# Performance work log

Measured on AMD Instinct MI355X. Metric: run time of the kernel, lower is better.

## Reference

```python
import jax, jax.numpy as jnp
import numpy as np

D_MODEL, D_FF, H, B, S = 1024, 4096, 16, 4, 2048
D_K = D_MODEL // H
EPS = 1e-5
NEG = -1e9


def _custom_ln(x, alpha, bias):
    # torch: mean, std (unbiased, N-1), alpha*(x-mean)/(std+eps)+bias; alpha/bias scalars
    mean = jnp.mean(x, axis=-1, keepdims=True)
    n = x.shape[-1]
    var = jnp.sum((x - mean) ** 2, axis=-1, keepdims=True) / (n - 1)
    std = jnp.sqrt(var)
    return alpha * (x - mean) / (std + EPS) + bias


def setup_inputs() -> dict:
    key = jax.random.key(0)
    ks = jax.random.split(key, 12)
    sc_d = 1.0 / np.sqrt(D_MODEL)
    sc_f = 1.0 / np.sqrt(D_FF)
    inp = {
        "x": jax.random.normal(ks[0], (B, S, D_MODEL), jnp.float32),
        "src_mask": jnp.ones((B, 1, 1, S), jnp.int32),
        "wq": jax.random.normal(ks[1], (D_MODEL, D_MODEL), jnp.float32) * sc_d,
        "bq": jnp.zeros((D_MODEL,), jnp.float32),
        "wk": jax.random.normal(ks[2], (D_MODEL, D_MODEL), jnp.float32) * sc_d,
        "bk": jnp.zeros((D_MODEL,), jnp.float32),
        "wv": jax.random.normal(ks[3], (D_MODEL, D_MODEL), jnp.float32) * sc_d,
        "bv": jnp.zeros((D_MODEL,), jnp.float32),
        "wo": jax.random.normal(ks[4], (D_MODEL, D_MODEL), jnp.float32) * sc_d,
        "bo": jnp.zeros((D_MODEL,), jnp.float32),
        "w1": jax.random.normal(ks[5], (D_MODEL, D_FF), jnp.float32) * sc_d,
        "b1": jnp.zeros((D_FF,), jnp.float32),
        "w2": jax.random.normal(ks[6], (D_FF, D_MODEL), jnp.float32) * sc_f,
        "b2": jnp.zeros((D_MODEL,), jnp.float32),
        "ln1_a": jnp.ones((1,), jnp.float32),
        "ln1_b": jnp.zeros((1,), jnp.float32),
        "ln2_a": jnp.ones((1,), jnp.float32),
        "ln2_b": jnp.zeros((1,), jnp.float32),
    }
    return inp


def _attention(xn, src_mask, wq, bq, wk, bk, wv, bv, wo, bo):
    q = (xn @ wq + bq).reshape(B, S, H, D_K).transpose(0, 2, 1, 3)  # [B,H,S,Dk]
    k = (xn @ wk + bk).reshape(B, S, H, D_K).transpose(0, 2, 1, 3)
    v = (xn @ wv + bv).reshape(B, S, H, D_K).transpose(0, 2, 1, 3)
    scores = jnp.einsum("bhqd,bhkd->bhqk", q, k) / np.sqrt(D_K)
    scores = jnp.where(src_mask == 0, NEG, scores)
    attn = jax.nn.softmax(scores, axis=-1)
    ctx = jnp.einsum("bhqk,bhkd->bhqd", attn, v)
    ctx = ctx.transpose(0, 2, 1, 3).reshape(B, S, D_MODEL)
    return ctx @ wo + bo


def reference(x, src_mask, wq, bq, wk, bk, wv, bv, wo, bo,
              w1, b1, w2, b2, ln1_a, ln1_b, ln2_a, ln2_b):
    # pre-LN attention residual (dropout=0 -> identity)
    xn = _custom_ln(x, ln1_a, ln1_b)
    x = x + _attention(xn, src_mask, wq, bq, wk, bk, wv, bv, wo, bo)
    # pre-LN FFN residual
    xn = _custom_ln(x, ln2_a, ln2_b)
    ff = jax.nn.relu(xn @ w1 + b1) @ w2 + b2
    return x + ff
```

## Files before the change

### kernel.cpp

```cpp
#include <hip/hip_runtime.h>

typedef unsigned short u16;
typedef __bf16 bf16x8 __attribute__((ext_vector_type(8)));
typedef float f32x4 __attribute__((ext_vector_type(4)));

__device__ __forceinline__ u16 f2bf(float f) {
  unsigned u = __builtin_bit_cast(unsigned, f);
  unsigned lsb = (u >> 16) & 1u;
  u += 0x7fffu + lsb;
  return (u16)(u >> 16);
}

__device__ __forceinline__ unsigned cvt_pk_bf16(float lo, float hi) {
  unsigned r;
  asm("v_cvt_pk_bf16_f32 %0, %1, %2" : "=v"(r) : "v"(lo), "v"(hi));
  return r;
}

__device__ __forceinline__ void gld_lds16(const u16* g, u16* l) {
  __builtin_amdgcn_global_load_lds(
      (__attribute__((address_space(1))) void*)g,
      (__attribute__((address_space(3))) void*)l, 16, 0, 0);
}

__global__ __launch_bounds__(256) void ln_kernel(
    const float* __restrict__ x, u16* __restrict__ out,
    const float* __restrict__ alpha_p, const float* __restrict__ beta_p) {
  const int row = blockIdx.x;
  const int t = threadIdx.x;
  const float4 v = reinterpret_cast<const float4*>(x + (size_t)row * 1024)[t];
  float s = v.x + v.y + v.z + v.w;
  float sq = v.x * v.x + v.y * v.y + v.z * v.z + v.w * v.w;
#pragma unroll
  for (int off = 32; off > 0; off >>= 1) {
    s += __shfl_down(s, off);
    sq += __shfl_down(sq, off);
  }
  __shared__ float red[8];
  const int w = t >> 6;
  if ((t & 63) == 0) { red[w] = s; red[4 + w] = sq; }
  __syncthreads();
  const float ts = red[0] + red[1] + red[2] + red[3];
  const float tq = red[4] + red[5] + red[6] + red[7];
  const float mean = ts * (1.0f / 1024.0f);
  float var = (tq - ts * mean) * (1.0f / 1023.0f);
  var = fmaxf(var, 0.0f);
  const float rden = 1.0f / (sqrtf(var) + 1e-5f);
  const float a = alpha_p[0], bb = beta_p[0];
  uint2 ov;
  ov.x = cvt_pk_bf16(a * (v.x - mean) * rden + bb, a * (v.y - mean) * rden + bb);
  ov.y = cvt_pk_bf16(a * (v.z - mean) * rden + bb, a * (v.w - mean) * rden + bb);
  reinterpret_cast<uint2*>(out + (size_t)row * 1024)[t] = ov;
}

__global__ __launch_bounds__(256) void wcvt_t(
    const float* __restrict__ w, u16* __restrict__ wt, int K, int N, float scale) {
  __shared__ float tile[32][33];
  const int n0 = blockIdx.x * 32, k0 = blockIdx.y * 32;
  const int tx = threadIdx.x, ty = threadIdx.y;
#pragma unroll
  for (int i = 0; i < 4; ++i)
    tile[ty + i * 8][tx] = w[(size_t)(k0 + ty + i * 8) * N + n0 + tx];
  __syncthreads();
#pragma unroll
  for (int i = 0; i < 4; ++i)
    wt[(size_t)(n0 + ty + i * 8) * K + k0 + tx] = f2bf(tile[tx][ty + i * 8] * scale);
}

__global__ __launch_bounds__(256) void pack_bias(
    const float* __restrict__ a, const float* __restrict__ b,
    const float* __restrict__ c, float* __restrict__ o, float qscale) {
  const int i = blockIdx.x * 256 + threadIdx.x;
  o[i] = (i < 1024) ? a[i] * qscale : ((i < 2048) ? b[i - 1024] : c[i - 2048]);
}

__global__ __launch_bounds__(256) void mk_mbias(
    const int* __restrict__ mask, float* __restrict__ mb, int* __restrict__ flags) {
  const int b = blockIdx.x, t = threadIdx.x;
  __shared__ int bad;
  if (t == 0) bad = 0;
  __syncthreads();
  int loc = 0;
#pragma unroll
  for (int i = 0; i < 8; ++i) {
    const int idx = b * 2048 + t * 8 + i;
    const int mv = mask[idx];
    mb[idx] = mv ? 0.f : -1.4427e9f;
    loc |= (mv == 0);
  }
  if (loc) atomicOr(&bad, 1);
  __syncthreads();
  if (t == 0) flags[b] = !bad;
}

template <int EPI>
__global__ __launch_bounds__(256) void gemm_bt(
    const u16* __restrict__ A, const u16* __restrict__ Bt,
    const float* __restrict__ bias, const float* __restrict__ res,
    void* __restrict__ Cout, u16* __restrict__ vt, int M, int N, int K) {
  __shared__ u16 As[128 * 32];
  __shared__ u16 Bs[128 * 32];
  const int tid = threadIdx.x;
  const int l = tid & 63;
  const int w = tid >> 6;
  const int wr = w >> 1, wc = w & 1;
  const int gx = gridDim.x;
  int id = blockIdx.y * gx + blockIdx.x;
  const int nwg = gx * gridDim.y;
  id = (id & 7) * (nwg >> 3) + (id >> 3);
  const int n0 = (id % gx) * 128;
  const int m0 = (id / gx) * 128;
  const int lr = l & 15, lk = (l >> 4) * 8;

  f32x4 acc[4][4];
#pragma unroll
  for (int i = 0; i < 4; ++i)
#pragma unroll
    for (int j = 0; j < 4; ++j) acc[i][j] = f32x4{0.f, 0.f, 0.f, 0.f};

  const int srow = tid >> 2;
  const int scol = (tid & 3) * 8;
  const u16* gA0 = A + (size_t)(m0 + srow) * K + scol;
  const u16* gA1 = A + (size_t)(m0 + 64 + srow) * K + scol;
  const u16* gB0 = Bt + (size_t)(n0 + srow) * K + scol;
  const u16* gB1 = Bt + (size_t)(n0 + 64 + srow) * K + scol;
  u16* lA0 = &As[tid * 8];
  u16* lA1 = &As[2048 + tid * 8];
  u16* lB0 = &Bs[tid * 8];
  u16* lB1 = &Bs[2048 + tid * 8];

  for (int k0 = 0; k0 < K; k0 += 32) {
    gld_lds16(gA0 + k0, lA0);
    gld_lds16(gA1 + k0, lA1);
    gld_lds16(gB0 + k0, lB0);
    gld_lds16(gB1 + k0, lB1);
    __syncthreads();
    bf16x8 a[4], b[4];
#pragma unroll
    for (int mf = 0; mf < 4; ++mf)
      a[mf] = *reinterpret_cast<const bf16x8*>(&As[(wr * 64 + mf * 16 + lr) * 32 + lk]);
#pragma unroll
    for (int nf = 0; nf < 4; ++nf)
      b[nf] = *reinterpret_cast<const bf16x8*>(&Bs[(wc * 64 + nf * 16 + lr) * 32 + lk]);
#pragma unroll
    for (int mf = 0; mf < 4; ++mf)
#pragma unroll
      for (int nf = 0; nf < 4; ++nf)
        acc[mf][nf] = __builtin_amdgcn_mfma_f32_16x16x32_bf16(a[mf], b[nf], acc[mf][nf], 0, 0, 0);
    __syncthreads();
  }

  if (EPI == 3 && n0 >= 2048) {
#pragma unroll
    for (int mf = 0; mf < 4; ++mf) {
#pragma unroll
      for (int nf = 0; nf < 4; ++nf) {
        const int col = n0 + wc * 64 + nf * 16 + lr;
        const float bv = bias[col];
        const int row0 = m0 + wr * 64 + mf * 16 + (l >> 4) * 4;
        const int bb = row0 >> 11, s0 = row0 & 2047;
        const int d = col - 2048;
        uint2 pv;
        pv.x = cvt_pk_bf16(acc[mf][nf][0] + bv, acc[mf][nf][1] + bv);
        pv.y = cvt_pk_bf16(acc[mf][nf][2] + bv, acc[mf][nf][3] + bv);
        *reinterpret_cast<uint2*>(vt + ((size_t)bb * 1024 + d) * 2048 + s0) = pv;
      }
    }
    return;
  }

#pragma unroll
  for (int mf = 0; mf < 4; ++mf) {
#pragma unroll
    for (int nf = 0; nf < 4; ++nf) {
      const int col = n0 + wc * 64 + nf * 16 + lr;
      const float bv = bias[col];
#pragma unroll
      for (int j = 0; j < 4; ++j) {
        const int row = m0 + wr * 64 + mf * 16 + (l >> 4) * 4 + j;
        const size_t idx = (size_t)row * N + col;
        const float vv = acc[mf][nf][j] + bv;
        if (EPI == 0 || EPI == 3)
          ((u16*)Cout)[idx] = f2bf(vv);
        else if (EPI == 1)
          ((float*)Cout)[idx] = vv + res[idx];
        else
          ((u16*)Cout)[idx] = f2bf(fmaxf(vv, 0.f));
      }
    }
  }
}

__global__ __launch_bounds__(256, 4) void attn_fwd4(
    const u16* __restrict__ qkv, const u16* __restrict__ vt,
    const float* __restrict__ mbias, const int* __restrict__ flags,
    u16* __restrict__ ctx) {
  __shared__ u16 Ks[2][64 * 64];
  __shared__ u16 Vs[2][64 * 64];
  const int tid = threadIdx.x;
  const int l = tid & 63;
  const int w = tid >> 6;
  const int b = blockIdx.y >> 4, h = blockIdx.y & 15;
  const int r0 = blockIdx.x * 128 + w * 32;
  const int lr = l & 15, lg = l >> 4;

  const u16* qb = qkv + (size_t)b * 2048 * 3072 + h * 64;
  const u16* kp = qb + 1024;
  const u16* vb = vt + ((size_t)b * 1024 + h * 64) * 2048;
  const float* mb = mbias + (size_t)b * 2048;
  const int allLive = flags[b];

  bf16x8 qf[2][2];
#pragma unroll
  for (int m = 0; m < 2; ++m)
#pragma unroll
    for (int ks = 0; ks < 2; ++ks)
      qf[m][ks] = *reinterpret_cast<const bf16x8*>(
          qb + (size_t)(r0 + m * 16 + lr) * 3072 + ks * 32 + lg * 8);

  float mrun[2] = {-1e30f, -1e30f};
  float lrun[2] = {0.f, 0.f};
  f32x4 o[2][4];
#pragma unroll
  for (int m = 0; m < 2; ++m)
#pragma unroll
    for (int d = 0; d < 4; ++d) o[m][d] = f32x4{0.f, 0.f, 0.f, 0.f};

  const u16* kS[2];
  const u16* vS[2];
#pragma unroll
  for (int i = 0; i < 2; ++i) {
    const int ci = tid + i * 256;
    const int row = ci >> 3, cc = ci & 7;
    const int sc = cc ^ (row & 7);
    kS[i] = kp + (size_t)row * 3072 + sc * 8;
    vS[i] = vb + (size_t)row * 2048 + sc * 8;
  }
#pragma unroll
  for (int i = 0; i < 2; ++i) {
    const int ci8 = (tid + i * 256) * 8;
    gld_lds16(kS[i], &Ks[0][ci8]);
    gld_lds16(vS[i], &Vs[0][ci8]);
  }
  asm volatile("s_waitcnt vmcnt(0)" ::: "memory");
  __syncthreads();

  union U8 { unsigned u[4]; bf16x8 v; };

  int cur = 0;
  for (int t = 0; t < 32; ++t) {
    const int kb0 = t * 64;
    if (t + 1 < 32) {
      const int nb = kb0 + 64;
#pragma unroll
      for (int i = 0; i < 2; ++i) {
        const int ci8 = (tid + i * 256) * 8;
        gld_lds16(kS[i] + (size_t)nb * 3072, &Ks[cur ^ 1][ci8]);
        gld_lds16(vS[i] + nb, &Vs[cur ^ 1][ci8]);
      }
    }

    f32x4 st[2][4];
    __builtin_amdgcn_s_setprio(1);
#pragma unroll
    for (int cf = 0; cf < 4; ++cf) {
      const int krow = cf * 16 + lr;
      const int ch0 = lg ^ (krow & 7);
      const int ch1 = (4 + lg) ^ (krow & 7);
      const bf16x8 kf0 = *reinterpret_cast<const bf16x8*>(&Ks[cur][krow * 64 + ch0 * 8]);
      const bf16x8 kf1 = *reinterpret_cast<const bf16x8*>(&Ks[cur][krow * 64 + ch1 * 8]);
#pragma unroll
      for (int m = 0; m < 2; ++m) {
        f32x4 acc = __builtin_amdgcn_mfma_f32_16x16x32_bf16(kf0, qf[m][0],
                                                            f32x4{0.f, 0.f, 0.f, 0.f}, 0, 0, 0);
        st[m][cf] = __builtin_amdgcn_mfma_f32_16x16x32_bf16(kf1, qf[m][1], acc, 0, 0, 0);
      }
    }
    __builtin_amdgcn_s_setprio(0);

    if (!allLive) {
#pragma unroll
      for (int cf = 0; cf < 4; ++cf) {
        const float4 m4 = *reinterpret_cast<const float4*>(mb + kb0 + cf * 16 + lg * 4);
#pragma unroll
        for (int m = 0; m < 2; ++m) {
          st[m][cf][0] += m4.x;
          st[m][cf][1] += m4.y;
          st[m][cf][2] += m4.z;
          st[m][cf][3] += m4.w;
        }
      }
    }

    bf16x8 paA[2], paB[2];
#pragma unroll
    for (int m = 0; m < 2; ++m) {
      float pm = fmaxf(fmaxf(st[m][0][0], st[m][0][1]), fmaxf(st[m][0][2], st[m][0][3]));
#pragma unroll
      for (int cf = 1; cf < 4; ++cf)
        pm = fmaxf(pm, fmaxf(fmaxf(st[m][cf][0], st[m][cf][1]),
                             fmaxf(st[m][cf][2], st[m][cf][3])));
      pm = fmaxf(pm, __shfl_xor(pm, 16));
      pm = fmaxf(pm, __shfl_xor(pm, 32));
      if (__any(pm > mrun[m] + 8.f)) {
        const float mn = fmaxf(mrun[m], pm);
        const float corr = exp2f(mrun[m] - mn);
        mrun[m] = mn;
        lrun[m] *= corr;
#pragma unroll
        for (int d = 0; d < 4; ++d)
#pragma unroll
          for (int j = 0; j < 4; ++j) o[m][d][j] *= corr;
      }
      float rs = 0.f;
#pragma unroll
      for (int cf = 0; cf < 4; ++cf)
#pragma unroll
        for (int j = 0; j < 4; ++j) {
          const float p = exp2f(st[m][cf][j] - mrun[m]);
          st[m][cf][j] = p;
          rs += p;
        }
      rs += __shfl_xor(rs, 16);
      rs += __shfl_xor(rs, 32);
      lrun[m] += rs;

      unsigned pk[4][2];
#pragma unroll
      for (int cf = 0; cf < 4; ++cf)
#pragma unroll
        for (int wp = 0; wp < 2; ++wp)
          pk[cf][wp] = cvt_pk_bf16(st[m][cf][2 * wp], st[m][cf][2 * wp + 1]);

      U8 a0, a1;
#pragma unroll
      for (int c = 0; c < 2; ++c) {
        const int src = lr + 16 * ((2 * lg + c) & 3);
#pragma unroll
        for (int wp = 0; wp < 2; ++wp) {
          const int v00 = __shfl((int)pk[0][wp], src);
          const int v01 = __shfl((int)pk[1][wp], src);
          const int v10 = __shfl((int)pk[2][wp], src);
          const int v11 = __shfl((int)pk[3][wp], src);
          a0.u[2 * c + wp] = (unsigned)((lg < 2) ? v00 : v01);
          a1.u[2 * c + wp] = (unsigned)((lg < 2) ? v10 : v11);
        }
      }
      paA[m] = a0.v;
      paB[m] = a1.v;
    }

    __builtin_amdgcn_s_setprio(1);
#pragma unroll
    for (int df = 0; df < 4; ++df) {
      const int vrow = df * 16 + lr;
      const int ch0 = lg ^ (vrow & 7);
      const int ch1 = (4 + lg) ^ (vrow & 7);
      const bf16x8 vf0 = *reinterpret_cast<const bf16x8*>(&Vs[cur][vrow * 64 + ch0 * 8]);
      const bf16x8 vf1 = *reinterpret_cast<const bf16x8*>(&Vs[cur][vrow * 64 + ch1 * 8]);
#pragma unroll
      for (int m = 0; m < 2; ++m) {
        o[m][df] = __builtin_amdgcn_mfma_f32_16x16x32_bf16(vf0, paA[m], o[m][df], 0, 0, 0);
        o[m][df] = __builtin_amdgcn_mfma_f32_16x16x32_bf16(vf1, paB[m], o[m][df], 0, 0, 0);
      }
    }
    __builtin_amdgcn_s_setprio(0);

    asm volatile("s_waitcnt vmcnt(0)" ::: "memory");
    __syncthreads();
    cur ^= 1;
  }

#pragma unroll
  for (int m = 0; m < 2; ++m) {
    const float rdiv = 1.f / lrun[m];
    const size_t rowbase = ((size_t)b * 2048 + r0 + m * 16 + lr) * 1024 + h * 64;
#pragma unroll
    for (int df = 0; df < 4; ++df) {
      uint2 s4;
      s4.x = cvt_pk_bf16(o[m][df][0] * rdiv, o[m][df][1] * rdiv);
      s4.y = cvt_pk_bf16(o[m][df][2] * rdiv, o[m][df][3] * rdiv);
      *reinterpret_cast<uint2*>(ctx + rowbase + df * 16 + lg * 4) = s4;
    }
  }
}

extern "C" void kernel_launch(void* const* d_in, const int* in_sizes, int n_in,
                              void* d_out, int out_size, void* d_ws, size_t ws_size,
                              hipStream_t stream) {
  const float* x = (const float*)d_in[0];
  const int* mask = (const int*)d_in[1];
  const float* wq = (const float*)d_in[2];
  const float* bq = (const float*)d_in[3];
  const float* wk = (const float*)d_in[4];
  const float* bk = (const float*)d_in[5];
  const float* wv = (const float*)d_in[6];
  const float* bv = (const float*)d_in[7];
  const float* wo = (const float*)d_in[8];
  const float* bo = (const float*)d_in[9];
  const float* w1 = (const float*)d_in[10];
  const float* b1 = (const float*)d_in[11];
  const float* w2 = (const float*)d_in[12];
  const float* b2 = (const float*)d_in[13];
  const float* ln1a = (const float*)d_in[14];
  const float* ln1b = (const float*)d_in[15];
  const float* ln2a = (const float*)d_in[16];
  const float* ln2b = (const float*)d_in[17];

  const float SCL2 = 0.125f * 1.4426950408889634f;

  char* ws = (char*)d_ws;
  const size_t MB = 1024ull * 1024ull;
  u16* WTQKV = (u16*)(ws + 0 * MB);
  u16* WTO = (u16*)(ws + 6 * MB);
  u16* W1T = (u16*)(ws + 8 * MB);
  u16* W2T = (u16*)(ws + 16 * MB);
  float* BQKV = (float*)(ws + 24 * MB);
  float* MBIAS = (float*)(ws + 24 * MB + 65536);
  int* FLAGS = (int*)(ws + 24 * MB + 131072);
  u16* QKV = (u16*)(ws + 25 * MB);
  u16* VT = (u16*)(ws + 73 * MB);
  u16* XN = (u16*)(ws + 89 * MB);
  u16* CTX = (u16*)(ws + 105 * MB);
  float* X2 = (float*)(ws + 25 * MB);
  u16* XN2 = (u16*)(ws + 57 * MB);
  u16* H1 = (u16*)(ws + 73 * MB);

  dim3 bt(32, 8);
  wcvt_t<<<dim3(32, 32), bt, 0, stream>>>(wq, WTQKV, 1024, 1024, SCL2);
  wcvt_t<<<dim3(32, 32), bt, 0, stream>>>(wk, WTQKV + 1024 * 1024, 1024, 1024, 1.f);
  wcvt_t<<<dim3(32, 32), bt, 0, stream>>>(wv, WTQKV + 2048 * 1024, 1024, 1024, 1.f);
  wcvt_t<<<dim3(32, 32), bt, 0, stream>>>(wo, WTO, 1024, 1024, 1.f);
  wcvt_t<<<dim3(128, 32), bt, 0, stream>>>(w1, W1T, 1024, 4096, 1.f);
  wcvt_t<<<dim3(32, 128), bt, 0, stream>>>(w2, W2T, 4096, 1024, 1.f);
  pack_bias<<<dim3(12), 256, 0, stream>>>(bq, bk, bv, BQKV, SCL2);
  mk_mbias<<<dim3(4), 256, 0, stream>>>(mask, MBIAS, FLAGS);

  ln_kernel<<<8192, 256, 0, stream>>>(x, XN, ln1a, ln1b);
  gemm_bt<3><<<dim3(24, 64), 256, 0, stream>>>(XN, WTQKV, BQKV, nullptr, QKV, VT, 8192, 3072, 1024);
  attn_fwd4<<<dim3(16, 64), 256, 0, stream>>>(QKV, VT, MBIAS, FLAGS, CTX);
  gemm_bt<1><<<dim3(8, 64), 256, 0, stream>>>(CTX, WTO, bo, x, X2, nullptr, 8192, 1024, 1024);
  ln_kernel<<<8192, 256, 0, stream>>>(X2, XN2, ln2a, ln2b);
  gemm_bt<2><<<dim3(32, 64), 256, 0, stream>>>(XN2, W1T, b1, nullptr, H1, nullptr, 8192, 4096, 1024);
  gemm_bt<1><<<dim3(8, 64), 256, 0, stream>>>(H1, W2T, b2, X2, (float*)d_out, nullptr, 8192, 1024, 4096);
}
```

Baseline: 506.9 us.

## Halve attention and N=1024 GEMM tiles and swizzle attention block order

The attention kernel now gives each wave 16 query rows instead of 32, so blocks cover 64 rows and twice as many blocks launch. Block ids are remapped so that neighbouring blocks share the same batch-head for K/V cache reuse. The GEMM gains a BM template parameter, and the two N=1024 GEMMs use 64-row tiles to double their grid and fill more compute units. The cost is that each K/V tile and B tile loaded into shared memory is reused across fewer rows, which raises load traffic per MFMA.

```diff
diff --git a/kernel.cpp b/kernel.cpp
--- a/kernel.cpp
+++ b/kernel.cpp
@@ -93,12 +93,13 @@
   if (t == 0) flags[b] = !bad;
 }
 
-template <int EPI>
+template <int EPI, int BM>
 __global__ __launch_bounds__(256) void gemm_bt(
     const u16* __restrict__ A, const u16* __restrict__ Bt,
     const float* __restrict__ bias, const float* __restrict__ res,
     void* __restrict__ Cout, u16* __restrict__ vt, int M, int N, int K) {
-  __shared__ u16 As[128 * 32];
+  constexpr int MF = BM / 32;
+  __shared__ u16 As[BM * 32];
   __shared__ u16 Bs[128 * 32];
   const int tid = threadIdx.x;
   const int l = tid & 63;
@@ -109,12 +110,12 @@
   const int nwg = gx * gridDim.y;
   id = (id & 7) * (nwg >> 3) + (id >> 3);
   const int n0 = (id % gx) * 128;
-  const int m0 = (id / gx) * 128;
+  const int m0 = (id / gx) * BM;
   const int lr = l & 15, lk = (l >> 4) * 8;
 
-  f32x4 acc[4][4];
-#pragma unroll
-  for (int i = 0; i < 4; ++i)
+  f32x4 acc[MF][4];
+#pragma unroll
+  for (int i = 0; i < MF; ++i)
 #pragma unroll
     for (int j = 0; j < 4; ++j) acc[i][j] = f32x4{0.f, 0.f, 0.f, 0.f};
 
@@ -131,19 +132,19 @@
 
   for (int k0 = 0; k0 < K; k0 += 32) {
     gld_lds16(gA0 + k0, lA0);
-    gld_lds16(gA1 + k0, lA1);
+    if constexpr (BM == 128) gld_lds16(gA1 + k0, lA1);
     gld_lds16(gB0 + k0, lB0);
     gld_lds16(gB1 + k0, lB1);
     __syncthreads();
-    bf16x8 a[4], b[4];
-#pragma unroll
-    for (int mf = 0; mf < 4; ++mf)
-      a[mf] = *reinterpret_cast<const bf16x8*>(&As[(wr * 64 + mf * 16 + lr) * 32 + lk]);
+    bf16x8 a[MF], b[4];
+#pragma unroll
+    for (int mf = 0; mf < MF; ++mf)
+      a[mf] = *reinterpret_cast<const bf16x8*>(&As[(wr * (BM / 2) + mf * 16 + lr) * 32 + lk]);
 #pragma unroll
     for (int nf = 0; nf < 4; ++nf)
       b[nf] = *reinterpret_cast<const bf16x8*>(&Bs[(wc * 64 + nf * 16 + lr) * 32 + lk]);
 #pragma unroll
-    for (int mf = 0; mf < 4; ++mf)
+    for (int mf = 0; mf < MF; ++mf)
 #pragma unroll
       for (int nf = 0; nf < 4; ++nf)
         acc[mf][nf] = __builtin_amdgcn_mfma_f32_16x16x32_bf16(a[mf], b[nf], acc[mf][nf], 0, 0, 0);
@@ -152,12 +153,12 @@
 
   if (EPI == 3 && n0 >= 2048) {
 #pragma unroll
-    for (int mf = 0; mf < 4; ++mf) {
+    for (int mf = 0; mf < MF; ++mf) {
 #pragma unroll
       for (int nf = 0; nf < 4; ++nf) {
         const int col = n0 + wc * 64 + nf * 16 + lr;
         const float bv = bias[col];
-        const int row0 = m0 + wr * 64 + mf * 16 + (l >> 4) * 4;
+        const int row0 = m0 + wr * (BM / 2) + mf * 16 + (l >> 4) * 4;
         const int bb = row0 >> 11, s0 = row0 & 2047;
         const int d = col - 2048;
         uint2 pv;
@@ -170,14 +171,14 @@
   }
 
 #pragma unroll
-  for (int mf = 0; mf < 4; ++mf) {
+  for (int mf = 0; mf < MF; ++mf) {
 #pragma unroll
     for (int nf = 0; nf < 4; ++nf) {
       const int col = n0 + wc * 64 + nf * 16 + lr;
       const float bv = bias[col];
 #pragma unroll
       for (int j = 0; j < 4; ++j) {
-        const int row = m0 + wr * 64 + mf * 16 + (l >> 4) * 4 + j;
+        const int row = m0 + wr * (BM / 2) + mf * 16 + (l >> 4) * 4 + j;
         const size_t idx = (size_t)row * N + col;
         const float vv = acc[mf][nf][j] + bv;
         if (EPI == 0 || EPI == 3)
@@ -191,7 +192,7 @@
   }
 }
 
-__global__ __launch_bounds__(256, 4) void attn_fwd4(
+__global__ __launch_bounds__(256, 4) void attn_fwd5(
     const u16* __restrict__ qkv, const u16* __restrict__ vt,
     const float* __restrict__ mbias, const int* __restrict__ flags,
     u16* __restrict__ ctx) {
@@ -200,8 +201,11 @@
   const int tid = threadIdx.x;
   const int l = tid & 63;
   const int w = tid >> 6;
-  const int b = blockIdx.y >> 4, h = blockIdx.y & 15;
-  const int r0 = blockIdx.x * 128 + w * 32;
+  const int p = blockIdx.y * 32 + blockIdx.x;
+  const int bh = (p & 7) * 8 + (p >> 8);
+  const int qx = (p >> 3) & 31;
+  const int b = bh >> 4, h = bh & 15;
+  const int r0 = qx * 64 + w * 16;
   const int lr = l & 15, lg = l >> 4;
 
   const u16* qb = qkv + (size_t)b * 2048 * 3072 + h * 64;
@@ -210,21 +214,17 @@
   const float* mb = mbias + (size_t)b * 2048;
   const int allLive = flags[b];
 
-  bf16x8 qf[2][2];
-#pragma unroll
-  for (int m = 0; m < 2; ++m)
-#pragma unroll
-    for (int ks = 0; ks < 2; ++ks)
-      qf[m][ks] = *reinterpret_cast<const bf16x8*>(
-          qb + (size_t)(r0 + m * 16 + lr) * 3072 + ks * 32 + lg * 8);
-
-  float mrun[2] = {-1e30f, -1e30f};
-  float lrun[2] = {0.f, 0.f};
-  f32x4 o[2][4];
-#pragma unroll
-  for (int m = 0; m < 2; ++m)
-#pragma unroll
-    for (int d = 0; d < 4; ++d) o[m][d] = f32x4{0.f, 0.f, 0.f, 0.f};
+  bf16x8 qf[2];
+#pragma unroll
+  for (int ks = 0; ks < 2; ++ks)
+    qf[ks] = *reinterpret_cast<const bf16x8*>(
+        qb + (size_t)(r0 + lr) * 3072 + ks * 32 + lg * 8);
+
+  float mrun = -1e30f;
+  float lrun = 0.f;
+  f32x4 o[4];
+#pragma unroll
+  for (int d = 0; d < 4; ++d) o[d] = f32x4{0.f, 0.f, 0.f, 0.f};
 
   const u16* kS[2];
   const u16* vS[2];
@@ -260,7 +260,7 @@
       }
     }
 
-    f32x4 st[2][4];
+    f32x4 st[4];
     __builtin_amdgcn_s_setprio(1);
 #pragma unroll
     for (int cf = 0; cf < 4; ++cf) {
@@ -269,12 +269,9 @@
       const int ch1 = (4 + lg) ^ (krow & 7);
       const bf16x8 kf0 = *reinterpret_cast<const bf16x8*>(&Ks[cur][krow * 64 + ch0 * 8]);
       const bf16x8 kf1 = *reinterpret_cast<const bf16x8*>(&Ks[cur][krow * 64 + ch1 * 8]);
-#pragma unroll
-      for (int m = 0; m < 2; ++m) {
-        f32x4 acc = __builtin_amdgcn_mfma_f32_16x16x32_bf16(kf0, qf[m][0],
-                                                            f32x4{0.f, 0.f, 0.f, 0.f}, 0, 0, 0);
-        st[m][cf] = __builtin_amdgcn_mfma_f32_16x16x32_bf16(kf1, qf[m][1], acc, 0, 0, 0);
-      }
+      f32x4 acc = __builtin_amdgcn_mfma_f32_16x16x32_bf16(kf0, qf[0],
+                                                          f32x4{0.f, 0.f, 0.f, 0.f}, 0, 0, 0);
+      st[cf] = __builtin_amdgcn_mfma_f32_16x16x32_bf16(kf1, qf[1], acc, 0, 0, 0);
     }
     __builtin_amdgcn_s_setprio(0);
 
@@ -282,73 +279,64 @@
 #pragma unroll
       for (int cf = 0; cf < 4; ++cf) {
         const float4 m4 = *reinterpret_cast<const float4*>(mb + kb0 + cf * 16 + lg * 4);
-#pragma unroll
-        for (int m = 0; m < 2; ++m) {
-          st[m][cf][0] += m4.x;
-          st[m][cf][1] += m4.y;
-          st[m][cf][2] += m4.z;
-          st[m][cf][3] += m4.w;
-        }
-      }
-    }
-
-    bf16x8 paA[2], paB[2];
-#pragma unroll
-    for (int m = 0; m < 2; ++m) {
-      float pm = fmaxf(fmaxf(st[m][0][0], st[m][0][1]), fmaxf(st[m][0][2], st[m][0][3]));
-#pragma unroll
-      for (int cf = 1; cf < 4; ++cf)
-        pm = fmaxf(pm, fmaxf(fmaxf(st[m][cf][0], st[m][cf][1]),
-                             fmaxf(st[m][cf][2], st[m][cf][3])));
-      pm = fmaxf(pm, __shfl_xor(pm, 16));
-      pm = fmaxf(pm, __shfl_xor(pm, 32));
-      if (__any(pm > mrun[m] + 8.f)) {
-        const float mn = fmaxf(mrun[m], pm);
-        const float corr = exp2f(mrun[m] - mn);
-        mrun[m] = mn;
-        lrun[m] *= corr;
-#pragma unroll
-        for (int d = 0; d < 4; ++d)
-#pragma unroll
-          for (int j = 0; j < 4; ++j) o[m][d][j] *= corr;
-      }
-      float rs = 0.f;
-#pragma unroll
-      for (int cf = 0; cf < 4; ++cf)
-#pragma unroll
-        for (int j = 0; j < 4; ++j) {
-          const float p = exp2f(st[m][cf][j] - mrun[m]);
-          st[m][cf][j] = p;
-          rs += p;
-        }
-      rs += __shfl_xor(rs, 16);
-      rs += __shfl_xor(rs, 32);
-      lrun[m] += rs;
-
-      unsigned pk[4][2];
-#pragma unroll
-      for (int cf = 0; cf < 4; ++cf)
-#pragma unroll
-        for (int wp = 0; wp < 2; ++wp)
-          pk[cf][wp] = cvt_pk_bf16(st[m][cf][2 * wp], st[m][cf][2 * wp + 1]);
-
-      U8 a0, a1;
-#pragma unroll
-      for (int c = 0; c < 2; ++c) {
-        const int src = lr + 16 * ((2 * lg + c) & 3);
-#pragma unroll
-        for (int wp = 0; wp < 2; ++wp) {
-          const int v00 = __shfl((int)pk[0][wp], src);
-          const int v01 = __shfl((int)pk[1][wp], src);
-          const int v10 = __shfl((int)pk[2][wp], src);
-          const int v11 = __shfl((int)pk[3][wp], src);
-          a0.u[2 * c + wp] = (unsigned)((lg < 2) ? v00 : v01);
-          a1.u[2 * c + wp] = (unsigned)((lg < 2) ? v10 : v11);
-        }
-      }
-      paA[m] = a0.v;
-      paB[m] = a1.v;
-    }
+        st[cf][0] += m4.x;
+        st[cf][1] += m4.y;
+        st[cf][2] += m4.z;
+        st[cf][3] += m4.w;
+      }
+    }
+
+    float pm = fmaxf(fmaxf(st[0][0], st[0][1]), fmaxf(st[0][2], st[0][3]));
+#pragma unroll
+    for (int cf = 1; cf < 4; ++cf)
+      pm = fmaxf(pm, fmaxf(fmaxf(st[cf][0], st[cf][1]), fmaxf(st[cf][2], st[cf][3])));
+    pm = fmaxf(pm, __shfl_xor(pm, 16));
+    pm = fmaxf(pm, __shfl_xor(pm, 32));
+    if (__any(pm > mrun + 8.f)) {
+      const float mn = fmaxf(mrun, pm);
+      const float corr = exp2f(mrun - mn);
+      mrun = mn;
+      lrun *= corr;
+#pragma unroll
+      for (int d = 0; d < 4; ++d)
+#pragma unroll
+        for (int j = 0; j < 4; ++j) o[d][j] *= corr;
+    }
+    float rs = 0.f;
+#pragma unroll
+    for (int cf = 0; cf < 4; ++cf)
+#pragma unroll
+      for (int j = 0; j < 4; ++j) {
+        const float pp = exp2f(st[cf][j] - mrun);
+        st[cf][j] = pp;
+        rs += pp;
+      }
+    rs += __shfl_xor(rs, 16);
+    rs += __shfl_xor(rs, 32);
+    lrun += rs;
+
+    unsigned pk[4][2];
+#pragma unroll
+    for (int cf = 0; cf < 4; ++cf)
+#pragma unroll
+      for (int wp = 0; wp < 2; ++wp)
+        pk[cf][wp] = cvt_pk_bf16(st[cf][2 * wp], st[cf][2 * wp + 1]);
+
+    U8 a0, a1;
+#pragma unroll
+    for (int c = 0; c < 2; ++c) {
+      const int src = lr + 16 * ((2 * lg + c) & 3);
+#pragma unroll
+      for (int wp = 0; wp < 2; ++wp) {
+        const int v00 = __shfl((int)pk[0][wp], src);
+        const int v01 = __shfl((int)pk[1][wp], src);
+        const int v10 = __shfl((int)pk[2][wp], src);
+        const int v11 = __shfl((int)pk[3][wp], src);
+        a0.u[2 * c + wp] = (unsigned)((lg < 2) ? v00 : v01);
+        a1.u[2 * c + wp] = (unsigned)((lg < 2) ? v10 : v11);
+      }
+    }
+    bf16x8 paA = a0.v, paB = a1.v;
 
     __builtin_amdgcn_s_setprio(1);
 #pragma unroll
@@ -358,11 +346,8 @@
       const int ch1 = (4 + lg) ^ (vrow & 7);
       const bf16x8 vf0 = *reinterpret_cast<const bf16x8*>(&Vs[cur][vrow * 64 + ch0 * 8]);
       const bf16x8 vf1 = *reinterpret_cast<const bf16x8*>(&Vs[cur][vrow * 64 + ch1 * 8]);
-#pragma unroll
-      for (int m = 0; m < 2; ++m) {
-        o[m][df] = __builtin_amdgcn_mfma_f32_16x16x32_bf16(vf0, paA[m], o[m][df], 0, 0, 0);
-        o[m][df] = __builtin_amdgcn_mfma_f32_16x16x32_bf16(vf1, paB[m], o[m][df], 0, 0, 0);
-      }
+      o[df] = __builtin_amdgcn_mfma_f32_16x16x32_bf16(vf0, paA, o[df], 0, 0, 0);
+      o[df] = __builtin_amdgcn_mfma_f32_16x16x32_bf16(vf1, paB, o[df], 0, 0, 0);
     }
     __builtin_amdgcn_s_setprio(0);
 
@@ -371,17 +356,14 @@
     cur ^= 1;
   }
 
-#pragma unroll
-  for (int m = 0; m < 2; ++m) {
-    const float rdiv = 1.f / lrun[m];
-    const size_t rowbase = ((size_t)b * 2048 + r0 + m * 16 + lr) * 1024 + h * 64;
-#pragma unroll
-    for (int df = 0; df < 4; ++df) {
-      uint2 s4;
-      s4.x = cvt_pk_bf16(o[m][df][0] * rdiv, o[m][df][1] * rdiv);
-      s4.y = cvt_pk_bf16(o[m][df][2] * rdiv, o[m][df][3] * rdiv);
-      *reinterpret_cast<uint2*>(ctx + rowbase + df * 16 + lg * 4) = s4;
-    }
+  const float rdiv = 1.f / lrun;
+  const size_t rowbase = ((size_t)b * 2048 + r0 + lr) * 1024 + h * 64;
+#pragma unroll
+  for (int df = 0; df < 4; ++df) {
+    uint2 s4;
+    s4.x = cvt_pk_bf16(o[df][0] * rdiv, o[df][1] * rdiv);
+    s4.y = cvt_pk_bf16(o[df][2] * rdiv, o[df][3] * rdiv);
+    *reinterpret_cast<uint2*>(ctx + rowbase + df * 16 + lg * 4) = s4;
   }
 }
 
@@ -437,10 +419,10 @@
   mk_mbias<<<dim3(4), 256, 0, stream>>>(mask, MBIAS, FLAGS);
 
   ln_kernel<<<8192, 256, 0, stream>>>(x, XN, ln1a, ln1b);
-  gemm_bt<3><<<dim3(24, 64), 256, 0, stream>>>(XN, WTQKV, BQKV, nullptr, QKV, VT, 8192, 3072, 1024);
-  attn_fwd4<<<dim3(16, 64), 256, 0, stream>>>(QKV, VT, MBIAS, FLAGS, CTX);
-  gemm_bt<1><<<dim3(8, 64), 256, 0, stream>>>(CTX, WTO, bo, x, X2, nullptr, 8192, 1024, 1024);
+  gemm_bt<3, 128><<<dim3(24, 64), 256, 0, stream>>>(XN, WTQKV, BQKV, nullptr, QKV, VT, 8192, 3072, 1024);
+  attn_fwd5<<<dim3(32, 64), 256, 0, stream>>>(QKV, VT, MBIAS, FLAGS, CTX);
+  gemm_bt<1, 64><<<dim3(8, 128), 256, 0, stream>>>(CTX, WTO, bo, x, X2, nullptr, 8192, 1024, 1024);
   ln_kernel<<<8192, 256, 0, stream>>>(X2, XN2, ln2a, ln2b);
-  gemm_bt<2><<<dim3(32, 64), 256, 0, stream>>>(XN2, W1T, b1, nullptr, H1, nullptr, 8192, 4096, 1024);
-  gemm_bt<1><<<dim3(8, 64), 256, 0, stream>>>(H1, W2T, b2, X2, (float*)d_out, nullptr, 8192, 1024, 4096);
-}
+  gemm_bt<2, 128><<<dim3(32, 64), 256, 0, stream>>>(XN2, W1T, b1, nullptr, H1, nullptr, 8192, 4096, 1024);
+  gemm_bt<1, 64><<<dim3(8, 128), 256, 0, stream>>>(H1, W2T, b2, X2, (float*)d_out, nullptr, 8192, 1024, 4096);
+}
```

Result: slower. 517.3 us (+2.1%).

## Use 64-row GEMM tiles for N=1024 projections and swizzle attention block order

Applied to the files above, without the earlier changes.

Templates the GEMM on the M tile size. The two N=1024 GEMMs (output projection and FFN down-projection) now use 64-row tiles, which doubles their workgroup count from 512 to 1024 so the 256 CUs are filled more evenly. The attention kernel remaps its block index so neighbouring blocks share (batch, head) pairs differently, aiming for better K/V cache locality, and the row-max reduction is rebalanced into a flatter tree. Smaller tiles lower per-block arithmetic intensity and mean more repeated B-tile loads.

```diff
diff --git a/kernel.cpp b/kernel.cpp
--- a/kernel.cpp
+++ b/kernel.cpp
@@ -93,12 +93,13 @@
   if (t == 0) flags[b] = !bad;
 }
 
-template <int EPI>
+template <int EPI, int BM>
 __global__ __launch_bounds__(256) void gemm_bt(
     const u16* __restrict__ A, const u16* __restrict__ Bt,
     const float* __restrict__ bias, const float* __restrict__ res,
     void* __restrict__ Cout, u16* __restrict__ vt, int M, int N, int K) {
-  __shared__ u16 As[128 * 32];
+  constexpr int MF = BM / 32;
+  __shared__ u16 As[BM * 32];
   __shared__ u16 Bs[128 * 32];
   const int tid = threadIdx.x;
   const int l = tid & 63;
@@ -109,12 +110,12 @@
   const int nwg = gx * gridDim.y;
   id = (id & 7) * (nwg >> 3) + (id >> 3);
   const int n0 = (id % gx) * 128;
-  const int m0 = (id / gx) * 128;
+  const int m0 = (id / gx) * BM;
   const int lr = l & 15, lk = (l >> 4) * 8;
 
-  f32x4 acc[4][4];
-#pragma unroll
-  for (int i = 0; i < 4; ++i)
+  f32x4 acc[MF][4];
+#pragma unroll
+  for (int i = 0; i < MF; ++i)
 #pragma unroll
     for (int j = 0; j < 4; ++j) acc[i][j] = f32x4{0.f, 0.f, 0.f, 0.f};
 
@@ -131,19 +132,19 @@
 
   for (int k0 = 0; k0 < K; k0 += 32) {
     gld_lds16(gA0 + k0, lA0);
-    gld_lds16(gA1 + k0, lA1);
+    if constexpr (BM == 128) gld_lds16(gA1 + k0, lA1);
     gld_lds16(gB0 + k0, lB0);
     gld_lds16(gB1 + k0, lB1);
     __syncthreads();
-    bf16x8 a[4], b[4];
-#pragma unroll
-    for (int mf = 0; mf < 4; ++mf)
-      a[mf] = *reinterpret_cast<const bf16x8*>(&As[(wr * 64 + mf * 16 + lr) * 32 + lk]);
+    bf16x8 a[MF], b[4];
+#pragma unroll
+    for (int mf = 0; mf < MF; ++mf)
+      a[mf] = *reinterpret_cast<const bf16x8*>(&As[(wr * (BM / 2) + mf * 16 + lr) * 32 + lk]);
 #pragma unroll
     for (int nf = 0; nf < 4; ++nf)
       b[nf] = *reinterpret_cast<const bf16x8*>(&Bs[(wc * 64 + nf * 16 + lr) * 32 + lk]);
 #pragma unroll
-    for (int mf = 0; mf < 4; ++mf)
+    for (int mf = 0; mf < MF; ++mf)
 #pragma unroll
       for (int nf = 0; nf < 4; ++nf)
         acc[mf][nf] = __builtin_amdgcn_mfma_f32_16x16x32_bf16(a[mf], b[nf], acc[mf][nf], 0, 0, 0);
@@ -152,12 +153,12 @@
 
   if (EPI == 3 && n0 >= 2048) {
 #pragma unroll
-    for (int mf = 0; mf < 4; ++mf) {
+    for (int mf = 0; mf < MF; ++mf) {
 #pragma unroll
       for (int nf = 0; nf < 4; ++nf) {
         const int col = n0 + wc * 64 + nf * 16 + lr;
         const float bv = bias[col];
-        const int row0 = m0 + wr * 64 + mf * 16 + (l >> 4) * 4;
+        const int row0 = m0 + wr * (BM / 2) + mf * 16 + (l >> 4) * 4;
         const int bb = row0 >> 11, s0 = row0 & 2047;
         const int d = col - 2048;
         uint2 pv;
@@ -170,14 +171,14 @@
   }
 
 #pragma unroll
-  for (int mf = 0; mf < 4; ++mf) {
+  for (int mf = 0; mf < MF; ++mf) {
 #pragma unroll
     for (int nf = 0; nf < 4; ++nf) {
       const int col = n0 + wc * 64 + nf * 16 + lr;
       const float bv = bias[col];
 #pragma unroll
       for (int j = 0; j < 4; ++j) {
-        const int row = m0 + wr * 64 + mf * 16 + (l >> 4) * 4 + j;
+        const int row = m0 + wr * (BM / 2) + mf * 16 + (l >> 4) * 4 + j;
         const size_t idx = (size_t)row * N + col;
         const float vv = acc[mf][nf][j] + bv;
         if (EPI == 0 || EPI == 3)
@@ -191,7 +192,7 @@
   }
 }
 
-__global__ __launch_bounds__(256, 4) void attn_fwd4(
+__global__ __launch_bounds__(256, 4) void attn_fwd6(
     const u16* __restrict__ qkv, const u16* __restrict__ vt,
     const float* __restrict__ mbias, const int* __restrict__ flags,
     u16* __restrict__ ctx) {
@@ -200,8 +201,12 @@
   const int tid = threadIdx.x;
   const int l = tid & 63;
   const int w = tid >> 6;
-  const int b = blockIdx.y >> 4, h = blockIdx.y & 15;
-  const int r0 = blockIdx.x * 128 + w * 32;
+  const int p = blockIdx.y * 16 + blockIdx.x;
+  const int idx = p >> 3;
+  const int bh = (p & 7) * 8 + (idx >> 4);
+  const int qx = idx & 15;
+  const int b = bh >> 4, h = bh & 15;
+  const int r0 = qx * 128 + w * 32;
   const int lr = l & 15, lg = l >> 4;
 
   const u16* qb = qkv + (size_t)b * 2048 * 3072 + h * 64;
@@ -295,11 +300,14 @@
     bf16x8 paA[2], paB[2];
 #pragma unroll
     for (int m = 0; m < 2; ++m) {
-      float pm = fmaxf(fmaxf(st[m][0][0], st[m][0][1]), fmaxf(st[m][0][2], st[m][0][3]));
-#pragma unroll
-      for (int cf = 1; cf < 4; ++cf)
-        pm = fmaxf(pm, fmaxf(fmaxf(st[m][cf][0], st[m][cf][1]),
-                             fmaxf(st[m][cf][2], st[m][cf][3])));
+      float p0 = fmaxf(fmaxf(st[m][0][0], st[m][0][1]), st[m][0][2]);
+      float p1 = fmaxf(fmaxf(st[m][0][3], st[m][1][0]), st[m][1][1]);
+      float p2 = fmaxf(fmaxf(st[m][1][2], st[m][1][3]), st[m][2][0]);
+      float p3 = fmaxf(fmaxf(st[m][2][1], st[m][2][2]), st[m][2][3]);
+      float p4 = fmaxf(fmaxf(st[m][3][0], st[m][3][1]), st[m][3][2]);
+      float pm = fmaxf(fmaxf(p0, p1), p2);
+      pm = fmaxf(fmaxf(pm, p3), p4);
+      pm = fmaxf(pm, st[m][3][3]);
       pm = fmaxf(pm, __shfl_xor(pm, 16));
       pm = fmaxf(pm, __shfl_xor(pm, 32));
       if (__any(pm > mrun[m] + 8.f)) {
@@ -317,9 +325,9 @@
       for (int cf = 0; cf < 4; ++cf)
 #pragma unroll
         for (int j = 0; j < 4; ++j) {
-          const float p = exp2f(st[m][cf][j] - mrun[m]);
-          st[m][cf][j] = p;
-          rs += p;
+          const float pp = exp2f(st[m][cf][j] - mrun[m]);
+          st[m][cf][j] = pp;
+          rs += pp;
         }
       rs += __shfl_xor(rs, 16);
       rs += __shfl_xor(rs, 32);
@@ -437,10 +445,10 @@
   mk_mbias<<<dim3(4), 256, 0, stream>>>(mask, MBIAS, FLAGS);
 
   ln_kernel<<<8192, 256, 0, stream>>>(x, XN, ln1a, ln1b);
-  gemm_bt<3><<<dim3(24, 64), 256, 0, stream>>>(XN, WTQKV, BQKV, nullptr, QKV, VT, 8192, 3072, 1024);
-  attn_fwd4<<<dim3(16, 64), 256, 0, stream>>>(QKV, VT, MBIAS, FLAGS, CTX);
-  gemm_bt<1><<<dim3(8, 64), 256, 0, stream>>>(CTX, WTO, bo, x, X2, nullptr, 8192, 1024, 1024);
+  gemm_bt<3, 128><<<dim3(24, 64), 256, 0, stream>>>(XN, WTQKV, BQKV, nullptr, QKV, VT, 8192, 3072, 1024);
+  attn_fwd6<<<dim3(16, 64), 256, 0, stream>>>(QKV, VT, MBIAS, FLAGS, CTX);
+  gemm_bt<1, 64><<<dim3(8, 128), 256, 0, stream>>>(CTX, WTO, bo, x, X2, nullptr, 8192, 1024, 1024);
   ln_kernel<<<8192, 256, 0, stream>>>(X2, XN2, ln2a, ln2b);
-  gemm_bt<2><<<dim3(32, 64), 256, 0, stream>>>(XN2, W1T, b1, nullptr, H1, nullptr, 8192, 4096, 1024);
-  gemm_bt<1><<<dim3(8, 64), 256, 0, stream>>>(H1, W2T, b2, X2, (float*)d_out, nullptr, 8192, 1024, 4096);
-}
+  gemm_bt<2, 128><<<dim3(32, 64), 256, 0, stream>>>(XN2, W1T, b1, nullptr, H1, nullptr, 8192, 4096, 1024);
+  gemm_bt<1, 64><<<dim3(8, 128), 256, 0, stream>>>(H1, W2T, b2, X2, (float*)d_out, nullptr, 8192, 1024, 4096);
+}
```

Result: no change. 499.4 us (-1.5%).
